# Performance work log

Measured on AMD Instinct MI355X. Metric: run time of the kernel, lower is better.

Reference implementation:

```python
import jax, jax.numpy as jnp
import numpy as np

IN_CH = 768
FH = FW = 14                      # hardcoded feature grid in the module
SCALES = (128.0, 256.0, 512.0)
RATIOS = (0.5, 1.0, 2.0)
A = len(SCALES) * len(RATIOS)     # 9 anchors / location
PRENMS_TOPK = 1000
NMS_THRESH = 0.7
TOPK = 300
MIN_SIZE = 16.0
BBOX_XFORM_CLIP = float(np.log(1000.0 / 16.0))


def generate_anchors(img_h, img_w):
    scales = jnp.asarray(SCALES, jnp.float32)
    ratios = jnp.asarray(RATIOS, jnp.float32)
    h_r = jnp.sqrt(ratios)
    w_r = 1.0 / h_r
    ws = (w_r[:, None] * scales[None, :]).reshape(-1)   # aspect-major, scale-minor
    hs = (h_r[:, None] * scales[None, :]).reshape(-1)
    base = jnp.round(jnp.stack([-ws, -hs, ws, hs], axis=1) / 2.0)  # [A,4]
    stride_h, stride_w = img_h // FH, img_w // FW
    sx = (jnp.arange(FW) * stride_w).astype(jnp.float32)
    sy = (jnp.arange(FH) * stride_h).astype(jnp.float32)
    yy, xx = jnp.meshgrid(sy, sx, indexing='ij')
    shifts = jnp.stack([xx, yy, xx, yy], axis=-1).reshape(-1, 4)   # [H*W,4]
    return (shifts[:, None, :] + base[None, :, :]).reshape(-1, 4)  # [H*W*A,4]


def decode_boxes(deltas, anchors):
    w = anchors[:, 2] - anchors[:, 0]
    h = anchors[:, 3] - anchors[:, 1]
    cx = anchors[:, 0] + 0.5 * w
    cy = anchors[:, 1] + 0.5 * h
    dx, dy = deltas[:, 0], deltas[:, 1]
    dw = jnp.minimum(deltas[:, 2], BBOX_XFORM_CLIP)
    dh = jnp.minimum(deltas[:, 3], BBOX_XFORM_CLIP)
    pcx = dx * w + cx
    pcy = dy * h + cy
    pw = jnp.exp(dw) * w
    ph = jnp.exp(dh) * h
    return jnp.stack([pcx - 0.5 * pw, pcy - 0.5 * ph,
                      pcx + 0.5 * pw, pcy + 0.5 * ph], axis=1)


def nms_keep(boxes, valid, thresh):
    # boxes sorted by descending score; greedy NMS. valid marks boxes that
    # survived the min-size filter.
    area = (boxes[:, 2] - boxes[:, 0]) * (boxes[:, 3] - boxes[:, 1])
    lt = jnp.maximum(boxes[:, None, :2], boxes[None, :, :2])
    rb = jnp.minimum(boxes[:, None, 2:], boxes[None, :, 2:])
    wh = jnp.clip(rb - lt, 0.0)
    inter = wh[..., 0] * wh[..., 1]
    union = area[:, None] + area[None, :] - inter
    iou = jnp.where(union > 0, inter / union, 0.0)   # [N,N]
    n = boxes.shape[0]
    order = jnp.arange(n)

    def body(i, keep):
        sup = (iou[i] > thresh) & keep[i] & (order > i)
        return keep & ~sup

    return jax.lax.fori_loop(0, n, body, valid)


def rpn_forward(image, feature, w_conv, b_conv, w_cls, b_cls, w_reg, b_reg):
    # feature: [1,197,768] -> drop CLS -> raw reshape to [1,768,14,14]
    feat = feature[:, 1:, :].reshape(1, IN_CH, FH, FW)
    x = jax.lax.conv_general_dilated(
        feat, w_conv, window_strides=(1, 1), padding='SAME',
        dimension_numbers=('NCHW', 'OIHW', 'NCHW')) + b_conv[None, :, None, None]
    x = jax.nn.relu(x)
    # 1x1 heads as einsum
    cls = jnp.einsum('nchw,oc->nohw', x, w_cls[:, :, 0, 0]) + b_cls[None, :, None, None]
    reg = jnp.einsum('nchw,oc->nohw', x, w_reg[:, :, 0, 0]) + b_reg[None, :, None, None]
    # [1,A,H,W] -> [H*W*A] (location-major, anchor-minor)
    scores = cls.transpose(0, 2, 3, 1).reshape(-1)
    # [1,4A,H,W] -> [1,A,4,H,W] -> [1,H,W,A,4] -> [H*W*A,4]
    deltas = reg.reshape(1, A, 4, FH, FW).transpose(0, 3, 4, 1, 2).reshape(-1, 4)

    img_h, img_w = image.shape[2], image.shape[3]
    anchors = generate_anchors(img_h, img_w)
    proposals = decode_boxes(deltas, anchors)

    # filter_proposals: sigmoid -> prenms topk -> clip -> min-size -> NMS -> topk
    probs = jax.nn.sigmoid(scores)
    k = min(PRENMS_TOPK, probs.shape[0])
    top_scores, idx = jax.lax.top_k(probs, k)
    boxes = proposals[idx]
    boxes = jnp.stack([jnp.clip(boxes[:, 0], 0.0, img_w),
                       jnp.clip(boxes[:, 1], 0.0, img_h),
                       jnp.clip(boxes[:, 2], 0.0, img_w),
                       jnp.clip(boxes[:, 3], 0.0, img_h)], axis=1)
    ws = boxes[:, 2] - boxes[:, 0]
    hs = boxes[:, 3] - boxes[:, 1]
    valid = (ws >= MIN_SIZE) & (hs >= MIN_SIZE)
    keep = nms_keep(boxes, valid, NMS_THRESH)

    masked = jnp.where(keep, top_scores, -1.0)   # sigmoid scores are > 0
    out_scores, oidx = jax.lax.top_k(masked, TOPK)
    out_boxes = boxes[oidx]
    pad = out_scores > 0.0                        # suppressed slots -> zero pad
    out_boxes = out_boxes * pad[:, None]
    out_scores = out_scores * pad
    return out_boxes, out_scores                  # [TOPK,4], [TOPK]


def setup_inputs() -> dict:
    key = jax.random.key(0)
    ks = jax.random.split(key, 6)
    return {
        'image': jax.random.normal(ks[0], (1, 3, 224, 224), jnp.float32),
        'feature': jax.random.normal(ks[1], (1, 197, IN_CH), jnp.float32),
        'w_conv': 0.01 * jax.random.normal(ks[2], (IN_CH, IN_CH, 3, 3), jnp.float32),
        'b_conv': jnp.zeros((IN_CH,), jnp.float32),
        'w_cls': 0.01 * jax.random.normal(ks[3], (A, IN_CH, 1, 1), jnp.float32),
        'b_cls': jnp.zeros((A,), jnp.float32),
        'w_reg': 0.01 * jax.random.normal(ks[4], (4 * A, IN_CH, 1, 1), jnp.float32),
        'b_reg': jnp.zeros((4 * A,), jnp.float32),
    }


def reference(image, feature, w_conv, b_conv, w_cls, b_cls, w_reg, b_reg):
    return rpn_forward(image, feature, w_conv, b_conv, w_cls, b_cls, w_reg, b_reg)
```

## Files before the change

### kernel.cpp

```cpp
#include <hip/hip_runtime.h>
#include <cstdint>
#include <cstddef>

#define IN_CH 768
#define FH 14
#define FW 14
#define NPOS 196
#define NA 9
#define NANCH 1764
#define K1 1000
#define TOPK_N 300
#define CSPLIT 16
#define CPBLK (IN_CH / CSPLIT)
#define WCH (CPBLK / 4)
#define HQ 8
#define HCC (IN_CH / HQ)
#define BBOX_CLIP 4.135166556742356f
#define IMG_W 224.0f
#define IMG_H 224.0f

typedef unsigned long long ull;

__device__ __forceinline__ uint32_t f2sort(float f) {
    uint32_t b = __float_as_uint(f);
    return (b & 0x80000000u) ? ~b : (b | 0x80000000u);
}
__device__ __forceinline__ float sort2f(uint32_t s) {
    uint32_t b = (s & 0x80000000u) ? (s & 0x7fffffffu) : ~s;
    return __uint_as_float(b);
}

__global__ __launch_bounds__(256) void k_pad(const float* __restrict__ feature,
                                             float* __restrict__ pad) {
    const int c = blockIdx.x, t = threadIdx.x;
    const int row = t >> 4, col = t & 15;
    const bool in = (row >= 1 && row <= 14 && col >= 1 && col <= 14);
    pad[(size_t)c * 256 + t] = in ? feature[IN_CH + (size_t)c * NPOS + (row - 1) * FW + (col - 1)] : 0.f;
}

__global__ __launch_bounds__(256) void k_conv(const float* __restrict__ pad,
                                              const float* __restrict__ w_conv,
                                              float* __restrict__ xpart) {
    __shared__ float wlds[CPBLK * 8 * 12];
    __shared__ float redbuf[8 * NPOS];
    const int tid  = threadIdx.x;
    const int wv   = tid >> 6, lane = tid & 63;
    const int cs   = blockIdx.x & (CSPLIT - 1);
    const int ob   = blockIdx.x / CSPLIT;
    const int o0   = ob * 8;

    for (int i = tid; i < CPBLK * 8 * 9; i += 256) {
        const int oo = i / (CPBLK * 9);
        const int r  = i % (CPBLK * 9);
        const int cc = r / 9, k = r % 9;
        wlds[(cc * 8 + oo) * 12 + k] =
            w_conv[((size_t)(o0 + oo) * IN_CH + (cs * CPBLK + cc)) * 9 + k];
    }

    const int row = lane >> 2, s4 = (lane & 3) * 4;
    const bool act = (row < FH);
    const int rr = act ? row : 0;

    const int cbase = cs * CPBLK + wv * WCH;
    const float* base = pad + (size_t)cbase * 256 + rr * 16 + s4;

    float acc[8][4];
#pragma unroll
    for (int oo = 0; oo < 8; oo++)
#pragma unroll
        for (int q = 0; q < 4; q++) acc[oo][q] = 0.f;

    float t[3][6];
#pragma unroll
    for (int rI = 0; rI < 3; rI++) {
        const float4 a = *(const float4*)(base + rI * 16);
        const float2 b = *(const float2*)(base + rI * 16 + 4);
        t[rI][0] = a.x; t[rI][1] = a.y; t[rI][2] = a.z; t[rI][3] = a.w;
        t[rI][4] = b.x; t[rI][5] = b.y;
    }

    __syncthreads();

    for (int cc = 0; cc < WCH; cc++) {
        float tn[3][6];
        if (cc + 1 < WCH) {
            const float* nb = base + (size_t)(cc + 1) * 256;
#pragma unroll
            for (int rI = 0; rI < 3; rI++) {
                const float4 a = *(const float4*)(nb + rI * 16);
                const float2 b = *(const float2*)(nb + rI * 16 + 4);
                tn[rI][0] = a.x; tn[rI][1] = a.y; tn[rI][2] = a.z; tn[rI][3] = a.w;
                tn[rI][4] = b.x; tn[rI][5] = b.y;
            }
        }
        const int cib = wv * WCH + cc;
#pragma unroll
        for (int oo = 0; oo < 8; oo++) {
            const int off = (cib * 8 + oo) * 12;
            const float4 wA = *(const float4*)&wlds[off];
            const float4 wB = *(const float4*)&wlds[off + 4];
            const float  w8 = wlds[off + 8];
#pragma unroll
            for (int k = 0; k < 4; k++) {
                acc[oo][k] += t[0][k] * wA.x + t[0][k + 1] * wA.y + t[0][k + 2] * wA.z
                            + t[1][k] * wA.w + t[1][k + 1] * wB.x + t[1][k + 2] * wB.y
                            + t[2][k] * wB.z + t[2][k + 1] * wB.w + t[2][k + 2] * w8;
            }
        }
        if (cc + 1 < WCH) {
#pragma unroll
            for (int rI = 0; rI < 3; rI++)
#pragma unroll
                for (int j = 0; j < 6; j++) t[rI][j] = tn[rI][j];
        }
    }

    __syncthreads();
    for (int w = 0; w < 4; w++) {
        if (wv == w && act) {
#pragma unroll
            for (int oo = 0; oo < 8; oo++)
#pragma unroll
                for (int k = 0; k < 4; k++) {
                    const int cx = s4 + k;
                    if (cx < FW) {
                        const int p = row * FW + cx;
                        if (w == 0) redbuf[oo * NPOS + p] = acc[oo][k];
                        else        redbuf[oo * NPOS + p] += acc[oo][k];
                    }
                }
        }
        __syncthreads();
    }
    for (int i = tid; i < 8 * NPOS; i += 256)
        xpart[((size_t)cs * IN_CH + o0 + (i / NPOS)) * NPOS + (i % NPOS)] = redbuf[i];
}

__global__ void k_reduce_relu(const float* __restrict__ xpart,
                              const float* __restrict__ b_conv,
                              float* __restrict__ xbuf) {
    const int f = blockIdx.x * blockDim.x + threadIdx.x;
    if (f >= IN_CH * NPOS) return;
    const int o = f / NPOS;
    float s = b_conv[o];
#pragma unroll
    for (int cs = 0; cs < CSPLIT; cs++) s += xpart[(size_t)cs * IN_CH * NPOS + f];
    xbuf[f] = fmaxf(s, 0.f);
}

__global__ __launch_bounds__(256) void k_heads(const float* __restrict__ xbuf,
                                               const float* __restrict__ w_cls,
                                               const float* __restrict__ w_reg,
                                               float* __restrict__ hpart) {
    const int ch = blockIdx.x % 45;
    const int q  = blockIdx.x / 45;
    const int p  = threadIdx.x;
    if (p >= NPOS) return;
    const float* w = (ch < NA) ? (w_cls + (size_t)ch * IN_CH)
                               : (w_reg + (size_t)(ch - NA) * IN_CH);
    float acc = 0.f;
    const int c0 = q * HCC;
#pragma unroll 8
    for (int c = c0; c < c0 + HCC; c++) acc += xbuf[(size_t)c * NPOS + p] * w[c];
    hpart[((size_t)q * 45 + ch) * NPOS + p] = acc;
}

__global__ __launch_bounds__(256) void k_select(const float* __restrict__ hpart,
                                                const float* __restrict__ b_cls,
                                                const float* __restrict__ b_reg,
                                                float* __restrict__ boxes1000,
                                                float* __restrict__ scores1000,
                                                unsigned* __restrict__ invalid) {
    __shared__ ull ks[NANCH];
    const int tid = threadIdx.x;

    for (int it = 0; it < 7; it++) {
        const int i = it * 256 + tid;
        if (i < NANCH) {
            const int p = i / NA, a = i % NA;
            float sc = b_cls[a];
#pragma unroll
            for (int q = 0; q < HQ; q++)
                sc += hpart[(size_t)q * 45 * NPOS + (size_t)a * NPOS + p];
            const float prob = 1.0f / (1.0f + expf(-sc));
            ks[i] = ((ull)(__float_as_uint(prob) | 0x80000000u) << 32)
                  | (ull)(0xFFFFFFFFu - (unsigned)i);
        }
    }
    __syncthreads();

    const int i = blockIdx.x * 256 + tid;
    const ull ki = (i < NANCH) ? ks[i] : 0ull;
    int rank = 0;
#pragma unroll 12
    for (int j = 0; j < NANCH; j++) rank += (ks[j] > ki) ? 1 : 0;

    if (i < NANCH && rank < K1) {
        const int p = i / NA, a = i % NA;
        const int yy = p / FW, xx = p % FW;
        const int r = a / 3, s = a % 3;
        const float scv = (s == 0) ? 128.f : ((s == 1) ? 256.f : 512.f);
        const float rat = (r == 0) ? 0.5f : ((r == 1) ? 1.0f : 2.0f);
        const float hr = sqrtf(rat), wr = 1.0f / hr;
        const float wsv = wr * scv, hsv = hr * scv;
        const float sxf = (float)(xx * 16), syf = (float)(yy * 16);
        const float ax0 = sxf + rintf(-0.5f * wsv);
        const float ay0 = syf + rintf(-0.5f * hsv);
        const float ax1 = sxf + rintf(0.5f * wsv);
        const float ay1 = syf + rintf(0.5f * hsv);
        const float w = ax1 - ax0, h = ay1 - ay0;
        const float cx = ax0 + 0.5f * w, cy = ay0 + 0.5f * h;
        const int rc0 = NA + (a * 4 + 0), rc1 = NA + (a * 4 + 1);
        const int rc2 = NA + (a * 4 + 2), rc3 = NA + (a * 4 + 3);
        float dx = b_reg[a * 4 + 0], dy = b_reg[a * 4 + 1];
        float dwv = b_reg[a * 4 + 2], dhv = b_reg[a * 4 + 3];
#pragma unroll
        for (int q = 0; q < HQ; q++) {
            const size_t base = (size_t)q * 45 * NPOS;
            dx  += hpart[base + (size_t)rc0 * NPOS + p];
            dy  += hpart[base + (size_t)rc1 * NPOS + p];
            dwv += hpart[base + (size_t)rc2 * NPOS + p];
            dhv += hpart[base + (size_t)rc3 * NPOS + p];
        }
        const float dw = fminf(dwv, BBOX_CLIP);
        const float dh = fminf(dhv, BBOX_CLIP);
        const float pcx = dx * w + cx, pcy = dy * h + cy;
        const float pw = expf(dw) * w, ph = expf(dh) * h;
        const float b0 = fminf(fmaxf(pcx - 0.5f * pw, 0.f), IMG_W);
        const float b1 = fminf(fmaxf(pcy - 0.5f * ph, 0.f), IMG_H);
        const float b2 = fminf(fmaxf(pcx + 0.5f * pw, 0.f), IMG_W);
        const float b3 = fminf(fmaxf(pcy + 0.5f * ph, 0.f), IMG_H);
        boxes1000[rank * 4 + 0] = b0; boxes1000[rank * 4 + 1] = b1;
        boxes1000[rank * 4 + 2] = b2; boxes1000[rank * 4 + 3] = b3;
        scores1000[rank] = __uint_as_float((unsigned)(ki >> 32) & 0x7FFFFFFFu);
        const float bw = b2 - b0, bh = b3 - b1;
        invalid[rank] = (bw >= 16.f && bh >= 16.f) ? 0u : 1u;
    }
}

__global__ __launch_bounds__(1024) void k_iou_mask(const float* __restrict__ boxes1000,
                                                   ull* __restrict__ mask) {
    const int i = blockIdx.x;
    const int j = threadIdx.x;
    const float ix0 = boxes1000[i * 4 + 0], iy0 = boxes1000[i * 4 + 1];
    const float ix1 = boxes1000[i * 4 + 2], iy1 = boxes1000[i * 4 + 3];
    const float areai = (ix1 - ix0) * (iy1 - iy0);
    bool pred = false;
    if (j < K1 && j > i) {
        const float jx0 = boxes1000[j * 4 + 0], jy0 = boxes1000[j * 4 + 1];
        const float jx1 = boxes1000[j * 4 + 2], jy1 = boxes1000[j * 4 + 3];
        const float areaj = (jx1 - jx0) * (jy1 - jy0);
        const float xx0 = fmaxf(ix0, jx0), yy0 = fmaxf(iy0, jy0);
        const float xx1 = fminf(ix1, jx1), yy1 = fminf(iy1, jy1);
        const float w = fmaxf(xx1 - xx0, 0.f), h = fmaxf(yy1 - yy0, 0.f);
        const float inter = w * h;
        const float uni = areai + areaj - inter;
        const float iou = (uni > 0.f) ? inter / uni : 0.f;
        pred = iou > 0.7f;
    }
    const ull m = __ballot(pred);
    if ((j & 63) == 0) mask[(size_t)i * 16 + (j >> 6)] = m;
}

__global__ __launch_bounds__(1024) void k_scan_out(const ull* __restrict__ mask,
                                                   const unsigned* __restrict__ invalid,
                                                   const float* __restrict__ scores1000,
                                                   const float* __restrict__ boxes1000,
                                                   float* __restrict__ out) {
    __shared__ ull mlds[8192];
    const int tid = threadIdx.x;
    const int wv = tid >> 6, lane = tid & 63;

    {
        const bool inv = (tid < K1) ? (invalid[tid] & 1u) : false;
        const ull bal = __ballot(inv);
        if (lane == 0) mlds[wv] = bal;
    }
    __syncthreads();
    ull remv = 0ull;
    if (tid < 64 && lane < 16) remv = mlds[lane];
    __syncthreads();

    for (int half = 0; half < 2; half++) {
        const int rbase = half * 512;
        const int nwords = (half == 0) ? 8192 : (K1 - 512) * 16;
        for (int k = tid; k < nwords; k += 1024) mlds[k] = mask[(size_t)rbase * 16 + k];
        __syncthreads();
        if (tid < 64) {
            for (int w = half * 8; w < half * 8 + 8; w++) {
                ull cur = __shfl(remv, w);
                const int bbase = w * 64;
                const int nb = (K1 - bbase < 64) ? (K1 - bbase) : 64;
                if (nb <= 0) continue;
#pragma unroll 8
                for (int b = 0; b < nb; b++) {
                    const int i = bbase + b;
                    const ull m_lane = mlds[(size_t)(i - rbase) * 16 + (lane & 15)];
                    const ull m_diag = mlds[(size_t)(i - rbase) * 16 + (i >> 6)];
                    const bool kept = ((cur >> b) & 1ull) == 0ull;
                    remv |= kept ? m_lane : 0ull;
                    cur  |= kept ? m_diag : 0ull;
                }
            }
        }
        __syncthreads();
    }
    if (tid < 64 && lane < 16) mlds[1024 + lane] = remv;
    __syncthreads();

    const int j = tid;
    ull kj = 0ull;
    if (j < K1) {
        const bool rem = (mlds[1024 + (j >> 6)] >> (j & 63)) & 1ull;
        const float m = rem ? -1.0f : scores1000[j];
        kj = ((ull)f2sort(m) << 32) | (ull)(0xFFFFFFFFu - (unsigned)j);
    }
    __syncthreads();
    if (j < K1) mlds[j] = kj;
    __syncthreads();

    if (j < K1) {
        int rank = 0;
#pragma unroll 8
        for (int t = 0; t < K1; t++) rank += (mlds[t] > kj) ? 1 : 0;
        if (rank < TOPK_N) {
            const float sc = sort2f((unsigned)(kj >> 32));
            const unsigned b = 0xFFFFFFFFu - (unsigned)(kj & 0xFFFFFFFFull);
            float o0 = 0.f, o1 = 0.f, o2 = 0.f, o3 = 0.f, os = 0.f;
            if (sc > 0.f) {
                o0 = boxes1000[b * 4 + 0]; o1 = boxes1000[b * 4 + 1];
                o2 = boxes1000[b * 4 + 2]; o3 = boxes1000[b * 4 + 3];
                os = sc;
            }
            out[rank * 4 + 0] = o0; out[rank * 4 + 1] = o1;
            out[rank * 4 + 2] = o2; out[rank * 4 + 3] = o3;
            out[1200 + rank] = os;
        }
    }
}

extern "C" void kernel_launch(void* const* d_in, const int* in_sizes, int n_in,
                              void* d_out, int out_size, void* d_ws, size_t ws_size,
                              hipStream_t stream) {
    const float* feature = (const float*)d_in[1];
    const float* w_conv  = (const float*)d_in[2];
    const float* b_conv  = (const float*)d_in[3];
    const float* w_cls   = (const float*)d_in[4];
    const float* b_cls   = (const float*)d_in[5];
    const float* w_reg   = (const float*)d_in[6];
    const float* b_reg   = (const float*)d_in[7];
    float* out = (float*)d_out;

    char* w = (char*)d_ws;
    float*    pad     = (float*)(w + 0);
    float*    xpart   = (float*)(w + 786432);
    float*    xbuf    = (float*)(w + 10420224);
    float*    hpart   = (float*)(w + 11022336);
    float*    boxes   = (float*)(w + 11304576);
    float*    scrs    = (float*)(w + 11320576);
    unsigned* inval   = (unsigned*)(w + 11324576);
    ull*      mask    = (ull*)  (w + 11328576);

    k_pad<<<IN_CH, 256, 0, stream>>>(feature, pad);
    k_conv<<<96 * CSPLIT, 256, 0, stream>>>(pad, w_conv, xpart);
    k_reduce_relu<<<(IN_CH * NPOS + 255) / 256, 256, 0, stream>>>(xpart, b_conv, xbuf);
    k_heads<<<45 * HQ, 256, 0, stream>>>(xbuf, w_cls, w_reg, hpart);
    k_select<<<7, 256, 0, stream>>>(hpart, b_cls, b_reg, boxes, scrs, inval);
    k_iou_mask<<<K1, 1024, 0, stream>>>(boxes, mask);
    k_scan_out<<<1, 1024, 0, stream>>>(mask, inval, scrs, boxes, out);
}
```

Baseline: 240.4 us.

## Restructure NMS mask scan with register diag shuffles and direct global row reads

The greedy NMS scan no longer stages the whole 1000x16 suppression mask in LDS in two halves. Each 64-box word is resolved within the wave: the diagonal mask words are prefetched into registers one word ahead and broadcast with shuffles, producing a kept bitmask. Lanes 0-15 then OR in the mask rows of kept boxes read directly from global memory. This removes the bulk LDS fill, its barriers and the serial LDS reads on the dependency chain, and shrinks LDS use. In exchange, only one wave streams the row words from global or L2 memory, which can add latency.

Measured after the change: 252.5 us. 1.05x slower.

```diff
diff --git a/kernel.cpp b/kernel.cpp
--- a/kernel.cpp
+++ b/kernel.cpp
@@ -267,62 +267,74 @@
                                                    const float* __restrict__ scores1000,
                                                    const float* __restrict__ boxes1000,
                                                    float* __restrict__ out) {
-    __shared__ ull mlds[8192];
+    __shared__ ull keys_s[1024];
+    __shared__ ull remw_s[16];
+    __shared__ ull bal_s[16];
     const int tid = threadIdx.x;
     const int wv = tid >> 6, lane = tid & 63;
 
     {
         const bool inv = (tid < K1) ? (invalid[tid] & 1u) : false;
         const ull bal = __ballot(inv);
-        if (lane == 0) mlds[wv] = bal;
-    }
-    __syncthreads();
-    ull remv = 0ull;
-    if (tid < 64 && lane < 16) remv = mlds[lane];
-    __syncthreads();
-
-    for (int half = 0; half < 2; half++) {
-        const int rbase = half * 512;
-        const int nwords = (half == 0) ? 8192 : (K1 - 512) * 16;
-        for (int k = tid; k < nwords; k += 1024) mlds[k] = mask[(size_t)rbase * 16 + k];
-        __syncthreads();
-        if (tid < 64) {
-            for (int w = half * 8; w < half * 8 + 8; w++) {
-                ull cur = __shfl(remv, w);
-                const int bbase = w * 64;
-                const int nb = (K1 - bbase < 64) ? (K1 - bbase) : 64;
-                if (nb <= 0) continue;
+        if (lane == 0) bal_s[wv] = bal;
+    }
+    __syncthreads();
+
+    if (tid < 64) {
+        ull remv = (lane < 16) ? bal_s[lane] : 0ull;
+
+        int i0 = lane;
+        int i0c = (i0 < K1) ? i0 : (K1 - 1);
+        ull diag_next = mask[(size_t)i0c * 16 + (i0c >> 6)];
+
+        for (int w = 0; w < 16; w++) {
+            const int bbase = w * 64;
+            const ull diagv = diag_next;
+            if (w + 1 < 16) {
+                const int iN = bbase + 64 + lane;
+                const int iNc = (iN < K1) ? iN : (K1 - 1);
+                diag_next = mask[(size_t)iNc * 16 + (iNc >> 6)];
+            }
+
+            ull cur = __shfl(remv, w);
+            ull kept = 0ull;
+#pragma unroll
+            for (int b = 0; b < 64; b++) {
+                const ull db = __shfl(diagv, b);
+                const bool kb = (((cur >> b) & 1ull) == 0ull) && (bbase + b < K1);
+                cur  |= kb ? db : 0ull;
+                kept |= kb ? (1ull << b) : 0ull;
+            }
+
+            if (lane < 16) {
+                const ull* mrow = mask + (size_t)bbase * 16 + lane;
 #pragma unroll 8
-                for (int b = 0; b < nb; b++) {
+                for (int b = 0; b < 64; b++) {
                     const int i = bbase + b;
-                    const ull m_lane = mlds[(size_t)(i - rbase) * 16 + (lane & 15)];
-                    const ull m_diag = mlds[(size_t)(i - rbase) * 16 + (i >> 6)];
-                    const bool kept = ((cur >> b) & 1ull) == 0ull;
-                    remv |= kept ? m_lane : 0ull;
-                    cur  |= kept ? m_diag : 0ull;
+                    const int ic = (i < K1) ? b : 0;
+                    const ull mv = mrow[(size_t)ic * 16];
+                    remv |= ((kept >> b) & 1ull) ? mv : 0ull;
                 }
             }
         }
-        __syncthreads();
-    }
-    if (tid < 64 && lane < 16) mlds[1024 + lane] = remv;
+        if (lane < 16) remw_s[lane] = remv;
+    }
     __syncthreads();
 
     const int j = tid;
     ull kj = 0ull;
     if (j < K1) {
-        const bool rem = (mlds[1024 + (j >> 6)] >> (j & 63)) & 1ull;
+        const bool rem = (remw_s[j >> 6] >> (j & 63)) & 1ull;
         const float m = rem ? -1.0f : scores1000[j];
         kj = ((ull)f2sort(m) << 32) | (ull)(0xFFFFFFFFu - (unsigned)j);
     }
-    __syncthreads();
-    if (j < K1) mlds[j] = kj;
+    keys_s[tid] = kj;
     __syncthreads();
 
     if (j < K1) {
         int rank = 0;
 #pragma unroll 8
-        for (int t = 0; t < K1; t++) rank += (mlds[t] > kj) ? 1 : 0;
+        for (int t = 0; t < K1; t++) rank += (keys_s[t] > kj) ? 1 : 0;
         if (rank < TOPK_N) {
             const float sc = sort2f((unsigned)(kj >> 32));
             const unsigned b = 0xFFFFFFFFu - (unsigned)(kj & 0xFFFFFFFFull);
```
